# Optimization experiments

Hardware: AMD Instinct MI355X
Metric: run time of the kernel (lower is better)

Reference implementation:

```python
import jax, jax.numpy as jnp
import numpy as np

V, C, T = 4096, 32, 512


def setup_inputs() -> dict:
    key = jax.random.key(0)
    ks = jax.random.split(key, 6)
    return {
        "x": jax.random.normal(ks[0], (V, C, T), dtype=jnp.float32),
        "U_1": jax.random.normal(ks[1], (V,), dtype=jnp.float32),
        "U_2": jax.random.normal(ks[2], (C, V), dtype=jnp.float32),
        "U_3": jax.random.normal(ks[3], (C,), dtype=jnp.float32),
        "b_e": jax.random.normal(ks[4], (C, T, T), dtype=jnp.float32),
        "V_e": jax.random.normal(ks[5], (T, T), dtype=jnp.float32),
    }


def reference(x, U_1, U_2, U_3, b_e, V_e):
    # x: (V, C, T)
    # lhs = (x.permute(2,1,0) @ U_1) @ U_2  -> (T, C) @ (C, V) = (T, V)
    tmp = jnp.einsum("vct,v->tc", x, U_1)          # (T, C)
    lhs = tmp @ U_2                                   # (T, V)
    # rhs = x.permute(2,0,1) @ U_3 -> (T, V)
    rhs = jnp.einsum("vct,c->tv", x, U_3)           # (T, V)
    product = rhs @ lhs.T                             # (T, T)
    # sigmoid(product + b_e) broadcasts to (C, T, T); V_e @ ... -> (C, T, T)
    E = jnp.einsum("ts,csr->ctr", V_e, jax.nn.sigmoid(product + b_e))
    # max-subtract / exp / sum over dim 1 == softmax over axis 1
    return jax.nn.softmax(E, axis=1)
```

## Files before the change

kernel.cpp:

```cpp
#include <hip/hip_runtime.h>

#define V_N 4096
#define C_N 32
#define T_N 512

typedef float f32x4 __attribute__((ext_vector_type(4)));
typedef __bf16 bf16x8 __attribute__((ext_vector_type(8)));

__device__ inline f32x4 fma4(f32x4 a, float b, f32x4 c) {
    f32x4 r;
    r.x = fmaf(a.x, b, c.x); r.y = fmaf(a.y, b, c.y);
    r.z = fmaf(a.z, b, c.z); r.w = fmaf(a.w, b, c.w);
    return r;
}

__global__ __launch_bounds__(256) void k_pre(const float* __restrict__ Ve,
                                             __bf16* __restrict__ VeHi,
                                             __bf16* __restrict__ VeLo) {
    int o = blockIdx.x * 256 + threadIdx.x;
    int e = o & 7, l = (o >> 3) & 63, tile = o >> 9;
    int kk = tile & 15, tt = tile >> 4;
    int t = tt * 16 + (l & 15);
    int k = kk * 32 + (l >> 4) * 8 + e;
    float v = Ve[(size_t)t * T_N + k];
    __bf16 h = (__bf16)v;
    VeHi[o] = h;
    VeLo[o] = (__bf16)(v - (float)h);
}

__global__ __launch_bounds__(256, 1) void k_rt(const float* __restrict__ x,
                                               const float* __restrict__ U1,
                                               const float* __restrict__ U2,
                                               const float* __restrict__ U3,
                                               float* __restrict__ partT,
                                               float* __restrict__ partG) {
    const int vc = blockIdx.x;
    const int tid = threadIdx.x;
    const int w = tid >> 6;
    const int l = tid & 63;
    const int v0 = vc * 16;

    __shared__ f32x4 lsum[2][4][2][64];

    float u3loc[8];
#pragma unroll
    for (int i = 0; i < 8; ++i) u3loc[i] = U3[w * 8 + i];

    f32x4 accT[8][2];
    f32x4 gacc[8][2];
#pragma unroll
    for (int i = 0; i < 8; ++i)
#pragma unroll
        for (int s = 0; s < 2; ++s) {
            accT[i][s] = (f32x4)0.f;
            gacc[i][s] = (f32x4)0.f;
        }

    const float* xplane0 = x + (size_t)v0 * (C_N * T_N);
#pragma unroll 1
    for (int vi = 0; vi < 16; ++vi) {
        const float* xp = xplane0 + (size_t)vi * (C_N * T_N);
        float u1 = U1[v0 + vi];
        int buf = vi & 1;
        f32x4 racc0 = (f32x4)0.f, racc1 = (f32x4)0.f;
#pragma unroll
        for (int j = 0; j < 16; ++j) {
            f32x4 xv = *(const f32x4*)(xp + (size_t)(w * 16 + j) * 256 + l * 4);
            int i = j >> 1;
            if ((j & 1) == 0) {
                accT[i][0] = fma4(xv, u1, accT[i][0]);
                racc0 = fma4(xv, u3loc[i], racc0);
            } else {
                accT[i][1] = fma4(xv, u1, accT[i][1]);
                racc1 = fma4(xv, u3loc[i], racc1);
            }
        }
        lsum[buf][w][0][l] = racc0;
        lsum[buf][w][1][l] = racc1;
        __syncthreads();
        f32x4 rhs0 = (lsum[buf][0][0][l] + lsum[buf][1][0][l]) +
                     (lsum[buf][2][0][l] + lsum[buf][3][0][l]);
        f32x4 rhs1 = (lsum[buf][0][1][l] + lsum[buf][1][1][l]) +
                     (lsum[buf][2][1][l] + lsum[buf][3][1][l]);
        float u2loc[8];
#pragma unroll
        for (int i = 0; i < 8; ++i)
            u2loc[i] = U2[(size_t)(w * 8 + i) * V_N + v0 + vi];
#pragma unroll
        for (int i = 0; i < 8; ++i) {
            gacc[i][0] = fma4(rhs0, u2loc[i], gacc[i][0]);
            gacc[i][1] = fma4(rhs1, u2loc[i], gacc[i][1]);
        }
    }

    const size_t pbase = (size_t)vc * (C_N * T_N);
#pragma unroll
    for (int i = 0; i < 8; ++i)
#pragma unroll
        for (int s = 0; s < 2; ++s) {
            size_t off = pbase + (size_t)(w * 8 + i) * T_N + s * 256 + l * 4;
            *(f32x4*)&partT[off] = accT[i][s];
            *(f32x4*)&partG[off] = gacc[i][s];
        }
}

__global__ __launch_bounds__(128) void k_red(const float* __restrict__ partT,
                                             const float* __restrict__ partG,
                                             float* __restrict__ tmpT,
                                             float* __restrict__ Gc) {
    __shared__ f32x4 red[16][8];
    int oid = threadIdx.x >> 3;
    int seg = threadIdx.x & 7;
    int o = blockIdx.x * 16 + oid;
    int isG = o >> 12;
    int oo = o & 4095;
    int c = oo >> 7;
    int tq = oo & 127;
    const float* src = isG ? partG : partT;
    size_t base = (size_t)c * T_N + tq * 4;
    f32x4 s = (f32x4)0.f;
#pragma unroll 4
    for (int vc = seg * 32; vc < seg * 32 + 32; ++vc)
        s += *(const f32x4*)&src[base + (size_t)vc * (C_N * T_N)];
    red[oid][seg] = s;
    __syncthreads();
    if (seg == 0) {
        f32x4 tot = red[oid][0];
#pragma unroll
        for (int k = 1; k < 8; ++k) tot += red[oid][k];
        float* dst = isG ? Gc : tmpT;
        *(f32x4*)&dst[c * T_N + tq * 4] = tot;
    }
}

__global__ __launch_bounds__(256) void k_P2(const float* __restrict__ Gc,
                                            const float* __restrict__ tmpT,
                                            float* __restrict__ P) {
    __shared__ float Gs[32][64];
    __shared__ float Ts[32][64];
    int rbase = blockIdx.x * 64, sbase = blockIdx.y * 64;
    int tid = threadIdx.x;
    int tx = tid & 15, ty = tid >> 4;
    for (int i = tid; i < 2048; i += 256) {
        int cc = i >> 6, j = i & 63;
        Gs[cc][j] = Gc[cc * T_N + sbase + j];
        Ts[cc][j] = tmpT[cc * T_N + rbase + j];
    }
    __syncthreads();
    float acc[4][4] = {};
#pragma unroll
    for (int cc = 0; cc < 32; ++cc) {
        float a[4], b[4];
#pragma unroll
        for (int i = 0; i < 4; ++i) a[i] = Gs[cc][ty * 4 + i];
#pragma unroll
        for (int j = 0; j < 4; ++j) b[j] = Ts[cc][tx * 4 + j];
#pragma unroll
        for (int i = 0; i < 4; ++i)
#pragma unroll
            for (int j = 0; j < 4; ++j) acc[i][j] = fmaf(a[i], b[j], acc[i][j]);
    }
#pragma unroll
    for (int i = 0; i < 4; ++i) {
        f32x4 vv = {acc[i][0], acc[i][1], acc[i][2], acc[i][3]};
        *(f32x4*)&P[(size_t)(sbase + ty * 4 + i) * T_N + rbase + tx * 4] = vv;
    }
}

__global__ __launch_bounds__(512, 4) void k_fused(const float* __restrict__ P,
                                                  const float* __restrict__ be,
                                                  const __bf16* __restrict__ VeHi,
                                                  const __bf16* __restrict__ VeLo,
                                                  float* __restrict__ out) {
    __shared__ __bf16 S[32][512];
    const int rbase = blockIdx.x * 32;
    const int c = blockIdx.y;
    const int tid = threadIdx.x;
    const size_t cTT = (size_t)c * T_N * T_N;

    {
        int r4 = (tid & 7) * 4;
        int s0 = tid >> 3;
        for (int i = 0; i < 8; ++i) {
            int s = i * 64 + s0;
            size_t off = (size_t)s * T_N + rbase + r4;
            f32x4 pv = *(const f32x4*)&P[off];
            f32x4 bv = *(const f32x4*)&be[cTT + off];
#pragma unroll
            for (int j = 0; j < 4; ++j) {
                float vv = pv[j] + bv[j];
                float sg = 1.0f / (1.0f + __expf(-vv));
                int rl = r4 + j;
                S[rl][s ^ ((rl & 7) << 3)] = (__bf16)sg;
            }
        }
    }
    __syncthreads();

    const int lane = tid & 63;
    const int w = tid >> 6;
    const int wt = w & 3;
    const int wr = w >> 2;
    const int lhi = lane >> 4;
    const int llo = lane & 15;

    const bf16x8* fragHi = (const bf16x8*)VeHi;
    const bf16x8* fragLo = (const bf16x8*)VeLo;

    f32x4 acc[8];
#pragma unroll
    for (int mi = 0; mi < 8; ++mi) acc[mi] = (f32x4)0.f;

    for (int k0 = 0; k0 < T_N; k0 += 32) {
        int rr = wr * 16 + llo;
        int g = (k0 >> 3) + lhi;
        bf16x8 b = *(const bf16x8*)&S[rr][(g ^ (rr & 7)) << 3];
#pragma unroll
        for (int mi = 0; mi < 8; ++mi) {
            int tile = (wt * 8 + mi) * 16 + (k0 >> 5);
            bf16x8 ah = fragHi[tile * 64 + lane];
            bf16x8 al = fragLo[tile * 64 + lane];
            acc[mi] = __builtin_amdgcn_mfma_f32_16x16x32_bf16(ah, b, acc[mi], 0, 0, 0);
            acc[mi] = __builtin_amdgcn_mfma_f32_16x16x32_bf16(al, b, acc[mi], 0, 0, 0);
        }
    }
    __syncthreads();

    float* red = (float*)&S[0][0];
    float gmax, gsum;

    {
        float m = -3.4e38f;
#pragma unroll
        for (int mi = 0; mi < 8; ++mi)
#pragma unroll
            for (int q = 0; q < 4; ++q) m = fmaxf(m, acc[mi][q]);
        m = fmaxf(m, __shfl_xor(m, 16));
        m = fmaxf(m, __shfl_xor(m, 32));
        if (lane < 16) red[wt * 32 + wr * 16 + llo] = m;
    }
    __syncthreads();
    {
        int col = wr * 16 + llo;
        gmax = fmaxf(fmaxf(red[col], red[32 + col]),
                     fmaxf(red[64 + col], red[96 + col]));
    }
    {
        float ssum = 0.f;
#pragma unroll
        for (int mi = 0; mi < 8; ++mi)
#pragma unroll
            for (int q = 0; q < 4; ++q) {
                float e = __expf(acc[mi][q] - gmax);
                acc[mi][q] = e;
                ssum += e;
            }
        ssum += __shfl_xor(ssum, 16);
        ssum += __shfl_xor(ssum, 32);
        if (lane < 16) red[128 + wt * 32 + wr * 16 + llo] = ssum;
    }
    __syncthreads();
    {
        int col = wr * 16 + llo;
        gsum = 1.0f / (red[128 + col] + red[128 + 32 + col] +
                       red[128 + 64 + col] + red[128 + 96 + col]);
    }
    {
        int rg = rbase + wr * 16 + llo;
#pragma unroll
        for (int mi = 0; mi < 8; ++mi)
#pragma unroll
            for (int q = 0; q < 4; ++q) {
                int t = wt * 128 + mi * 16 + lhi * 4 + q;
                out[cTT + (size_t)t * T_N + rg] = acc[mi][q] * gsum;
            }
    }
}

extern "C" void kernel_launch(void* const* d_in, const int* in_sizes, int n_in,
                              void* d_out, int out_size, void* d_ws, size_t ws_size,
                              hipStream_t stream) {
    const float* x  = (const float*)d_in[0];
    const float* U1 = (const float*)d_in[1];
    const float* U2 = (const float*)d_in[2];
    const float* U3 = (const float*)d_in[3];
    const float* be = (const float*)d_in[4];
    const float* Ve = (const float*)d_in[5];
    float* out = (float*)d_out;

    float* ws    = (float*)d_ws;
    float* partT = ws;
    float* partG = ws + 4194304;
    float* P     = ws + 8388608;
    __bf16* VeHi = (__bf16*)(ws + 8650752);
    __bf16* VeLo = (__bf16*)(ws + 8781824);
    float* tmpT  = ws + 8912896;
    float* Gc    = ws + 8929280;

    k_pre <<<1024, 256, 0, stream>>>(Ve, VeHi, VeLo);
    k_rt  <<<256, 256, 0, stream>>>(x, U1, U2, U3, partT, partG);
    k_red <<<512, 128, 0, stream>>>(partT, partG, tmpT, Gc);
    k_P2  <<<dim3(8, 8), 256, 0, stream>>>(Gc, tmpT, P);
    k_fused<<<dim3(16, C_N), 512, 0, stream>>>(P, be, VeHi, VeLo, out);
}
```

Baseline: 123.6 us.

## Fuse Ve bf16 split into x-reduction kernel and split T across two blocks

Merges the Ve hi/lo bf16 preprocessing kernel into the main x-streaming kernel as extra blocks, saving one launch. The x reduction now splits each 16-vertex chunk across two blocks by T half, which doubles the grid to 512 working blocks and allows two blocks per CU. It also adds register double-buffering, so loads for the next vertex plane are issued before the barrier. Each block now handles half the columns, so the per-vertex U2 loads and LDS syncs are duplicated across the two blocks.

```diff
diff --git a/kernel.cpp b/kernel.cpp
--- a/kernel.cpp
+++ b/kernel.cpp
@@ -14,94 +14,103 @@
     return r;
 }
 
-__global__ __launch_bounds__(256) void k_pre(const float* __restrict__ Ve,
-                                             __bf16* __restrict__ VeHi,
-                                             __bf16* __restrict__ VeLo) {
-    int o = blockIdx.x * 256 + threadIdx.x;
-    int e = o & 7, l = (o >> 3) & 63, tile = o >> 9;
-    int kk = tile & 15, tt = tile >> 4;
-    int t = tt * 16 + (l & 15);
-    int k = kk * 32 + (l >> 4) * 8 + e;
-    float v = Ve[(size_t)t * T_N + k];
-    __bf16 h = (__bf16)v;
-    VeHi[o] = h;
-    VeLo[o] = (__bf16)(v - (float)h);
-}
-
-__global__ __launch_bounds__(256, 1) void k_rt(const float* __restrict__ x,
-                                               const float* __restrict__ U1,
-                                               const float* __restrict__ U2,
-                                               const float* __restrict__ U3,
-                                               float* __restrict__ partT,
-                                               float* __restrict__ partG) {
-    const int vc = blockIdx.x;
+__global__ __launch_bounds__(256, 2) void k_rtpre(const float* __restrict__ x,
+                                                  const float* __restrict__ U1,
+                                                  const float* __restrict__ U2,
+                                                  const float* __restrict__ U3,
+                                                  float* __restrict__ partT,
+                                                  float* __restrict__ partG,
+                                                  const float* __restrict__ Ve,
+                                                  __bf16* __restrict__ VeHi,
+                                                  __bf16* __restrict__ VeLo) {
+    __shared__ f32x4 lsum[2][4][64];
+
+    if (blockIdx.x >= 512) {
+        int o = (blockIdx.x - 512) * 256 + threadIdx.x;
+        int e = o & 7, lp = (o >> 3) & 63, tile = o >> 9;
+        int kk = tile & 15, tt = tile >> 4;
+        int t = tt * 16 + (lp & 15);
+        int k = kk * 32 + (lp >> 4) * 8 + e;
+        float v = Ve[(size_t)t * T_N + k];
+        __bf16 h = (__bf16)v;
+        VeHi[o] = h;
+        VeLo[o] = (__bf16)(v - (float)h);
+        return;
+    }
+
+    const int vc = blockIdx.x >> 1;
+    const int half = blockIdx.x & 1;
     const int tid = threadIdx.x;
     const int w = tid >> 6;
     const int l = tid & 63;
     const int v0 = vc * 16;
 
-    __shared__ f32x4 lsum[2][4][2][64];
-
     float u3loc[8];
 #pragma unroll
     for (int i = 0; i < 8; ++i) u3loc[i] = U3[w * 8 + i];
 
-    f32x4 accT[8][2];
-    f32x4 gacc[8][2];
-#pragma unroll
-    for (int i = 0; i < 8; ++i)
-#pragma unroll
-        for (int s = 0; s < 2; ++s) {
-            accT[i][s] = (f32x4)0.f;
-            gacc[i][s] = (f32x4)0.f;
-        }
-
-    const float* xplane0 = x + (size_t)v0 * (C_N * T_N);
-#pragma unroll 1
-    for (int vi = 0; vi < 16; ++vi) {
-        const float* xp = xplane0 + (size_t)vi * (C_N * T_N);
-        float u1 = U1[v0 + vi];
-        int buf = vi & 1;
-        f32x4 racc0 = (f32x4)0.f, racc1 = (f32x4)0.f;
-#pragma unroll
-        for (int j = 0; j < 16; ++j) {
-            f32x4 xv = *(const f32x4*)(xp + (size_t)(w * 16 + j) * 256 + l * 4);
-            int i = j >> 1;
-            if ((j & 1) == 0) {
-                accT[i][0] = fma4(xv, u1, accT[i][0]);
-                racc0 = fma4(xv, u3loc[i], racc0);
-            } else {
-                accT[i][1] = fma4(xv, u1, accT[i][1]);
-                racc1 = fma4(xv, u3loc[i], racc1);
-            }
-        }
-        lsum[buf][w][0][l] = racc0;
-        lsum[buf][w][1][l] = racc1;
+    f32x4 accT[8], gacc[8];
+#pragma unroll
+    for (int i = 0; i < 8; ++i) { accT[i] = (f32x4)0.f; gacc[i] = (f32x4)0.f; }
+
+    const float* xbase = x + (size_t)v0 * (C_N * T_N) + half * 256 + l * 4;
+
+#define LOADP(vi, X) { const float* xp_ = xbase + (size_t)(vi) * (C_N * T_N); \
+    _Pragma("unroll") for (int i_ = 0; i_ < 8; ++i_) \
+        X[i_] = *(const f32x4*)(xp_ + (size_t)(w * 8 + i_) * T_N); }
+
+    f32x4 A[8], B[8];
+    LOADP(0, A);
+#pragma unroll
+    for (int vi = 0; vi < 16; vi += 2) {
+        {
+            float u1 = U1[v0 + vi];
+            f32x4 racc = (f32x4)0.f;
+#pragma unroll
+            for (int i = 0; i < 8; ++i) {
+                accT[i] = fma4(A[i], u1, accT[i]);
+                racc = fma4(A[i], u3loc[i], racc);
+            }
+            lsum[0][w][l] = racc;
+        }
+        if (vi + 1 < 16) LOADP(vi + 1, B);
         __syncthreads();
-        f32x4 rhs0 = (lsum[buf][0][0][l] + lsum[buf][1][0][l]) +
-                     (lsum[buf][2][0][l] + lsum[buf][3][0][l]);
-        f32x4 rhs1 = (lsum[buf][0][1][l] + lsum[buf][1][1][l]) +
-                     (lsum[buf][2][1][l] + lsum[buf][3][1][l]);
-        float u2loc[8];
-#pragma unroll
-        for (int i = 0; i < 8; ++i)
-            u2loc[i] = U2[(size_t)(w * 8 + i) * V_N + v0 + vi];
-#pragma unroll
-        for (int i = 0; i < 8; ++i) {
-            gacc[i][0] = fma4(rhs0, u2loc[i], gacc[i][0]);
-            gacc[i][1] = fma4(rhs1, u2loc[i], gacc[i][1]);
-        }
-    }
-
-    const size_t pbase = (size_t)vc * (C_N * T_N);
-#pragma unroll
-    for (int i = 0; i < 8; ++i)
-#pragma unroll
-        for (int s = 0; s < 2; ++s) {
-            size_t off = pbase + (size_t)(w * 8 + i) * T_N + s * 256 + l * 4;
-            *(f32x4*)&partT[off] = accT[i][s];
-            *(f32x4*)&partG[off] = gacc[i][s];
-        }
+        {
+            f32x4 rhs = (lsum[0][0][l] + lsum[0][1][l]) +
+                        (lsum[0][2][l] + lsum[0][3][l]);
+#pragma unroll
+            for (int i = 0; i < 8; ++i)
+                gacc[i] = fma4(rhs, U2[(size_t)(w * 8 + i) * V_N + v0 + vi], gacc[i]);
+        }
+        {
+            float u1 = U1[v0 + vi + 1];
+            f32x4 racc = (f32x4)0.f;
+#pragma unroll
+            for (int i = 0; i < 8; ++i) {
+                accT[i] = fma4(B[i], u1, accT[i]);
+                racc = fma4(B[i], u3loc[i], racc);
+            }
+            lsum[1][w][l] = racc;
+        }
+        if (vi + 2 < 16) LOADP(vi + 2, A);
+        __syncthreads();
+        {
+            f32x4 rhs = (lsum[1][0][l] + lsum[1][1][l]) +
+                        (lsum[1][2][l] + lsum[1][3][l]);
+#pragma unroll
+            for (int i = 0; i < 8; ++i)
+                gacc[i] = fma4(rhs, U2[(size_t)(w * 8 + i) * V_N + v0 + vi + 1], gacc[i]);
+        }
+    }
+#undef LOADP
+
+    const size_t pbase = (size_t)vc * (C_N * T_N) + half * 256 + l * 4;
+#pragma unroll
+    for (int i = 0; i < 8; ++i) {
+        size_t off = pbase + (size_t)(w * 8 + i) * T_N;
+        *(f32x4*)&partT[off] = accT[i];
+        *(f32x4*)&partG[off] = gacc[i];
+    }
 }
 
 __global__ __launch_bounds__(128) void k_red(const float* __restrict__ partT,
@@ -297,8 +306,7 @@
     float* tmpT  = ws + 8912896;
     float* Gc    = ws + 8929280;
 
-    k_pre <<<1024, 256, 0, stream>>>(Ve, VeHi, VeLo);
-    k_rt  <<<256, 256, 0, stream>>>(x, U1, U2, U3, partT, partG);
+    k_rtpre<<<1536, 256, 0, stream>>>(x, U1, U2, U3, partT, partG, Ve, VeHi, VeLo);
     k_red <<<512, 128, 0, stream>>>(partT, partG, tmpT, Gc);
     k_P2  <<<dim3(8, 8), 256, 0, stream>>>(Gc, tmpT, P);
     k_fused<<<dim3(16, C_N), 512, 0, stream>>>(P, be, VeHi, VeLo, out);
```

Measured after the change: 252.0 us. 2.04x slower.

## Replace partial-sum buffers and reduction kernel with atomic accumulation; fold Ve split into main kernel

Applied to the files above, without the earlier changes.

Each k_rt block used to write its 32x512 partial sums for tmpT and Gc to a large workspace, and a separate kernel then reduced them. Now the blocks atomically add straight into the zeroed final arrays, and the Ve bf16 hi/lo split runs as extra blocks of the same launch. This removes about 32 MB of partial-sum writes and reads plus one launch, and it adds a small zeroing kernel. In exchange, 256 blocks contend on the same 32K addresses with scalar atomics, and the summation order is no longer deterministic.

```diff
diff --git a/kernel.cpp b/kernel.cpp
--- a/kernel.cpp
+++ b/kernel.cpp
@@ -14,33 +14,40 @@
     return r;
 }
 
-__global__ __launch_bounds__(256) void k_pre(const float* __restrict__ Ve,
-                                             __bf16* __restrict__ VeHi,
-                                             __bf16* __restrict__ VeLo) {
-    int o = blockIdx.x * 256 + threadIdx.x;
-    int e = o & 7, l = (o >> 3) & 63, tile = o >> 9;
-    int kk = tile & 15, tt = tile >> 4;
-    int t = tt * 16 + (l & 15);
-    int k = kk * 32 + (l >> 4) * 8 + e;
-    float v = Ve[(size_t)t * T_N + k];
-    __bf16 h = (__bf16)v;
-    VeHi[o] = h;
-    VeLo[o] = (__bf16)(v - (float)h);
-}
-
-__global__ __launch_bounds__(256, 1) void k_rt(const float* __restrict__ x,
-                                               const float* __restrict__ U1,
-                                               const float* __restrict__ U2,
-                                               const float* __restrict__ U3,
-                                               float* __restrict__ partT,
-                                               float* __restrict__ partG) {
+__global__ __launch_bounds__(256) void k_zero(float* __restrict__ zz) {
+    int i = (blockIdx.x * 256 + threadIdx.x) * 4;
+    *(f32x4*)&zz[i] = (f32x4)0.f;
+}
+
+__global__ __launch_bounds__(256, 1) void k_rtpre(const float* __restrict__ x,
+                                                  const float* __restrict__ U1,
+                                                  const float* __restrict__ U2,
+                                                  const float* __restrict__ U3,
+                                                  float* __restrict__ tmpT,
+                                                  float* __restrict__ Gc,
+                                                  const float* __restrict__ Ve,
+                                                  __bf16* __restrict__ VeHi,
+                                                  __bf16* __restrict__ VeLo) {
+    __shared__ f32x4 lsum[2][4][2][64];
+
+    if (blockIdx.x >= 256) {
+        int o = (blockIdx.x - 256) * 256 + threadIdx.x;
+        int e = o & 7, lp = (o >> 3) & 63, tile = o >> 9;
+        int kk = tile & 15, tt = tile >> 4;
+        int t = tt * 16 + (lp & 15);
+        int k = kk * 32 + (lp >> 4) * 8 + e;
+        float v = Ve[(size_t)t * T_N + k];
+        __bf16 h = (__bf16)v;
+        VeHi[o] = h;
+        VeLo[o] = (__bf16)(v - (float)h);
+        return;
+    }
+
     const int vc = blockIdx.x;
     const int tid = threadIdx.x;
     const int w = tid >> 6;
     const int l = tid & 63;
     const int v0 = vc * 16;
-
-    __shared__ f32x4 lsum[2][4][2][64];
 
     float u3loc[8];
 #pragma unroll
@@ -93,44 +100,17 @@
         }
     }
 
-    const size_t pbase = (size_t)vc * (C_N * T_N);
 #pragma unroll
     for (int i = 0; i < 8; ++i)
 #pragma unroll
         for (int s = 0; s < 2; ++s) {
-            size_t off = pbase + (size_t)(w * 8 + i) * T_N + s * 256 + l * 4;
-            *(f32x4*)&partT[off] = accT[i][s];
-            *(f32x4*)&partG[off] = gacc[i][s];
-        }
-}
-
-__global__ __launch_bounds__(128) void k_red(const float* __restrict__ partT,
-                                             const float* __restrict__ partG,
-                                             float* __restrict__ tmpT,
-                                             float* __restrict__ Gc) {
-    __shared__ f32x4 red[16][8];
-    int oid = threadIdx.x >> 3;
-    int seg = threadIdx.x & 7;
-    int o = blockIdx.x * 16 + oid;
-    int isG = o >> 12;
-    int oo = o & 4095;
-    int c = oo >> 7;
-    int tq = oo & 127;
-    const float* src = isG ? partG : partT;
-    size_t base = (size_t)c * T_N + tq * 4;
-    f32x4 s = (f32x4)0.f;
-#pragma unroll 4
-    for (int vc = seg * 32; vc < seg * 32 + 32; ++vc)
-        s += *(const f32x4*)&src[base + (size_t)vc * (C_N * T_N)];
-    red[oid][seg] = s;
-    __syncthreads();
-    if (seg == 0) {
-        f32x4 tot = red[oid][0];
-#pragma unroll
-        for (int k = 1; k < 8; ++k) tot += red[oid][k];
-        float* dst = isG ? Gc : tmpT;
-        *(f32x4*)&dst[c * T_N + tq * 4] = tot;
-    }
+            int base = (w * 8 + i) * T_N + s * 256 + l * 4;
+#pragma unroll
+            for (int q = 0; q < 4; ++q) {
+                atomicAdd(&tmpT[base + q], accT[i][s][q]);
+                atomicAdd(&Gc[base + q], gacc[i][s][q]);
+            }
+        }
 }
 
 __global__ __launch_bounds__(256) void k_P2(const float* __restrict__ Gc,
@@ -289,17 +269,14 @@
     float* out = (float*)d_out;
 
     float* ws    = (float*)d_ws;
-    float* partT = ws;
-    float* partG = ws + 4194304;
-    float* P     = ws + 8388608;
-    __bf16* VeHi = (__bf16*)(ws + 8650752);
-    __bf16* VeLo = (__bf16*)(ws + 8781824);
-    float* tmpT  = ws + 8912896;
-    float* Gc    = ws + 8929280;
-
-    k_pre <<<1024, 256, 0, stream>>>(Ve, VeHi, VeLo);
-    k_rt  <<<256, 256, 0, stream>>>(x, U1, U2, U3, partT, partG);
-    k_red <<<512, 128, 0, stream>>>(partT, partG, tmpT, Gc);
-    k_P2  <<<dim3(8, 8), 256, 0, stream>>>(Gc, tmpT, P);
+    float* tmpT  = ws;
+    float* Gc    = ws + 16384;
+    float* P     = ws + 32768;
+    __bf16* VeHi = (__bf16*)(ws + 294912);
+    __bf16* VeLo = (__bf16*)(ws + 425984);
+
+    k_zero <<<32, 256, 0, stream>>>(ws);
+    k_rtpre<<<256 + 1024, 256, 0, stream>>>(x, U1, U2, U3, tmpT, Gc, Ve, VeHi, VeLo);
+    k_P2   <<<dim3(8, 8), 256, 0, stream>>>(Gc, tmpT, P);
     k_fused<<<dim3(16, C_N), 512, 0, stream>>>(P, be, VeHi, VeLo, out);
 }
```

New measurement: 353.3 us. 2.86x slower.
